# Optimization experiments

Hardware: AMD Instinct MI355X
Metric: run time of the kernel (lower is better)

Reference implementation:

```python
import jax, jax.numpy as jnp
import numpy as np

N = 50000      # nodes
E = 800000     # edges (avg degree 16)
D_IN, D_H, D_OUT = 128, 256, 128


def setup_inputs() -> dict:
    key = jax.random.key(0)
    ks = jax.random.split(key, 12)
    x = jax.random.normal(ks[0], (N, D_IN), jnp.float32)
    src = jax.random.randint(ks[1], (E,), 0, N)
    dst = jax.random.randint(ks[2], (E,), 0, N)

    def lin(k, din, dout):
        return (jax.random.normal(k, (din, dout), jnp.float32) / np.sqrt(din)).astype(jnp.float32)

    dims = [(D_IN, D_H), (D_H, D_H), (D_H, D_OUT)]
    params = {}
    ki = 3
    for i, (di, do) in enumerate(dims):
        params[f"W_self{i}"] = lin(ks[ki], di, do); ki += 1
        params[f"W_neigh{i}"] = lin(ks[ki], di, do); ki += 1
        params[f"b{i}"] = jnp.zeros((do,), jnp.float32)
    return {"x": x, "src": src, "dst": dst, **params}


def _mean_agg(h, src, dst):
    # gather src features along edges, segment-mean into dst nodes
    msg = jnp.take(h, src, axis=0)                              # [E, D]
    s = jax.ops.segment_sum(msg, dst, num_segments=N)           # [N, D]
    deg = jax.ops.segment_sum(jnp.ones((dst.shape[0], 1), h.dtype), dst, num_segments=N)
    return s / jnp.maximum(deg, 1.0)                            # zero-degree -> 0, as in DGL


def reference(x, src, dst,
              W_self0, W_neigh0, b0,
              W_self1, W_neigh1, b1,
              W_self2, W_neigh2, b2):
    Ws = [(W_self0, W_neigh0, b0), (W_self1, W_neigh1, b1), (W_self2, W_neigh2, b2)]
    h = x
    for i, (Ws_i, Wn_i, b_i) in enumerate(Ws):
        neigh = _mean_agg(h, src, dst)
        h = h @ Ws_i + neigh @ Wn_i + b_i                       # SAGEConv('mean')
        if i < len(Ws) - 1:
            h = jax.nn.relu(h)                                  # activation between layers
    return h
```

## Files before the change

### kernel.cpp

```cpp
#include <hip/hip_runtime.h>

#define NN 50000
#define NE 800000
#define NCHK 200
#define CHKE 4000
#define NBUK 196
#define BCAP 5120
#define NOFF (NBUK * NCHK)
#define NSB  ((NOFF + 255) / 256)

typedef __attribute__((ext_vector_type(8))) short short8;
typedef __attribute__((ext_vector_type(4))) float f32x4;
typedef unsigned int u32;
typedef unsigned short u16;

__device__ __forceinline__ float bf2f(short u) {
    union { unsigned int i; float f; } c;
    c.i = ((unsigned int)(unsigned short)u) << 16;
    return c.f;
}
__device__ __forceinline__ short f2bf(float f) {
    union { float f; unsigned int i; } c; c.f = f;
    unsigned int u = c.i;
    unsigned int r = (u + 0x7FFFu + ((u >> 16) & 1u)) >> 16;
    return (short)r;
}


__global__ void cvt_f32_bf16_kernel(const float* __restrict__ in, short* __restrict__ out, int n) {
    int gid = blockIdx.x * 256 + threadIdx.x;
    if (gid < n) out[gid] = f2bf(in[gid]);
}

__global__ void wcvt_all_kernel(const float* __restrict__ Ws0, const float* __restrict__ Wn0,
                                const float* __restrict__ Ws1, const float* __restrict__ Wn1,
                                const float* __restrict__ Ws2, const float* __restrict__ Wn2,
                                short* __restrict__ wts) {
    int gid = blockIdx.x * 256 + threadIdx.x;
    const float* W; int K, Dout, base, loc;
    if (gid < 65536)       { K = 128; Dout = 256; base = (gid < 32768)  ? 0 : 32768;
                             W = (gid < 32768)  ? Ws0 : Wn0; loc = gid & 32767; }
    else if (gid < 196608) { K = 256; Dout = 256; base = (gid < 131072) ? 65536 : 131072;
                             W = (gid < 131072) ? Ws1 : Wn1; loc = (gid - 65536) & 65535; }
    else                   { K = 256; Dout = 128; base = (gid < 229376) ? 196608 : 229376;
                             W = (gid < 229376) ? Ws2 : Wn2; loc = (gid - 196608) & 32767; }
    int k = loc / Dout, d = loc - k * Dout;
    int kt = k >> 6, ks = (k >> 5) & 1, kg = (k >> 3) & 3, j = k & 7;
    int cgp = d >> 4, l = d & 15;
    int off = ((((kt * 2 + ks) * (Dout >> 4) + cgp) * 4 + kg) * 16 + l) * 8 + j;
    wts[base + off] = f2bf(W[(long)k * Dout + d]);
}

__global__ __launch_bounds__(256) void bucket_hist_kernel(const int* __restrict__ dst,
                                                          int* __restrict__ chist) {
    __shared__ int lh[NBUK];
    int b = blockIdx.x, t = threadIdx.x;
    for (int i = t; i < NBUK; i += 256) lh[i] = 0;
    __syncthreads();
    int base = b * CHKE;
    for (int i = t; i < CHKE; i += 256) atomicAdd(&lh[dst[base + i] >> 8], 1);
    __syncthreads();
    for (int i = t; i < NBUK; i += 256) chist[i * NCHK + b] = lh[i];
}

__global__ __launch_bounds__(256) void off_blocksum_kernel(const int* __restrict__ in,
                                                           int* __restrict__ bsum) {
    __shared__ int sm[256];
    int t = threadIdx.x;
    int idx = blockIdx.x * 256 + t;
    sm[t] = (idx < NOFF) ? in[idx] : 0;
    __syncthreads();
    for (int off = 128; off > 0; off >>= 1) {
        if (t < off) sm[t] += sm[t + off];
        __syncthreads();
    }
    if (t == 0) bsum[blockIdx.x] = sm[0];
}

__global__ __launch_bounds__(256) void off_scanb_kernel(const int* __restrict__ bsum,
                                                        int* __restrict__ bpre) {
    __shared__ int sm[256];
    int t = threadIdx.x;
    sm[t] = (t < NSB) ? bsum[t] : 0;
    __syncthreads();
    for (int o = 1; o < 256; o <<= 1) {
        int v = sm[t];
        int a = (t >= o) ? sm[t - o] : 0;
        __syncthreads();
        sm[t] = v + a;
        __syncthreads();
    }
    if (t < NSB) bpre[t] = (t == 0) ? 0 : sm[t - 1];
}

__global__ __launch_bounds__(256) void off_scatter_kernel(const int* __restrict__ in,
                                                          const int* __restrict__ bpre,
                                                          int* __restrict__ off) {
    __shared__ int sm[256];
    int t = threadIdx.x;
    int idx = blockIdx.x * 256 + t;
    int val = (idx < NOFF) ? in[idx] : 0;
    sm[t] = val;
    __syncthreads();
    for (int o = 1; o < 256; o <<= 1) {
        int v = sm[t];
        int a = (t >= o) ? sm[t - o] : 0;
        __syncthreads();
        sm[t] = v + a;
        __syncthreads();
    }
    if (idx < NOFF) off[idx] = bpre[blockIdx.x] + sm[t] - val;
}

__global__ __launch_bounds__(256) void bucket_scatter_kernel(const int* __restrict__ src,
                                                             const int* __restrict__ dst,
                                                             const int* __restrict__ off,
                                                             u32* __restrict__ ebuf) {
    __shared__ int lcur[NBUK];
    int b = blockIdx.x, t = threadIdx.x;
    for (int i = t; i < NBUK; i += 256) lcur[i] = off[i * NCHK + b];
    __syncthreads();
    int base = b * CHKE;
    for (int i = t; i < CHKE; i += 256) {
        int d = dst[base + i], s = src[base + i];
        int slot = atomicAdd(&lcur[d >> 8], 1);
        ebuf[slot] = ((u32)(d & 255) << 16) | (u32)s;
    }
}

__global__ __launch_bounds__(256) void bucket_sort_kernel(const u32* __restrict__ ebuf,
                                                          const int* __restrict__ off,
                                                          u16* __restrict__ srcs16,
                                                          int* __restrict__ row_start,
                                                          int* __restrict__ cnt) {
    __shared__ u32 earr[BCAP];
    __shared__ u16 s16[BCAP];
    __shared__ int lhist[256], lpre[256], lcur[256];
    int k = blockIdx.x, t = threadIdx.x;
    int base = off[k * NCHK];
    int end  = (k < NBUK - 1) ? off[(k + 1) * NCHK] : NE;
    int nE = end - base;
    lhist[t] = 0;
    __syncthreads();
    for (int i = t; i < nE; i += 256) {
        u32 e = ebuf[base + i];
        earr[i] = e;
        atomicAdd(&lhist[e >> 16], 1);
    }
    __syncthreads();
    int v = lhist[t];
    lpre[t] = v;
    __syncthreads();
    for (int o = 1; o < 256; o <<= 1) {
        int x = lpre[t];
        int a = (t >= o) ? lpre[t - o] : 0;
        __syncthreads();
        lpre[t] = x + a;
        __syncthreads();
    }
    int excl = lpre[t] - v;
    int node = k * 256 + t;
    if (node < NN) { row_start[node] = base + excl; cnt[node] = v; }
    lcur[t] = excl;
    __syncthreads();
    for (int i = t; i < nE; i += 256) {
        u32 e = earr[i];
        int pos = atomicAdd(&lcur[e >> 16], 1);
        s16[pos] = (u16)(e & 0xFFFFu);
    }
    __syncthreads();
    for (int i = t; i < nE; i += 256) srcs16[base + i] = s16[i];
}


template<int STRIDE_G>
__global__ __launch_bounds__(256) void gather_mean3_kernel(
    const short* __restrict__ h, const u16* __restrict__ srcs,
    const int* __restrict__ row_start, const int* __restrict__ cnt,
    short* __restrict__ nb)
{
    constexpr int EPL = 4;
    const int wave = threadIdx.x >> 6;
    const int lane = threadIdx.x & 63;
    const int v = blockIdx.x * 4 + wave;
    if (v >= NN) return;
    const int go = blockIdx.y * 16;
    const int c  = cnt[v];
    const int rs = row_start[v];
    const int slot = lane >> 4;
    const int cg   = (lane & 15) + go;
    float acc[8];
    #pragma unroll
    for (int j = 0; j < 8; ++j) acc[j] = 0.f;
    const short8* hp = (const short8*)h;
    int i = slot;
    for (; i + 3 * EPL < c; i += 4 * EPL) {
        int s0 = srcs[rs + i];
        int s1 = srcs[rs + i + EPL];
        int s2 = srcs[rs + i + 2 * EPL];
        int s3 = srcs[rs + i + 3 * EPL];
        short8 v0 = hp[(size_t)s0 * STRIDE_G + cg];
        short8 v1 = hp[(size_t)s1 * STRIDE_G + cg];
        short8 v2 = hp[(size_t)s2 * STRIDE_G + cg];
        short8 v3 = hp[(size_t)s3 * STRIDE_G + cg];
        #pragma unroll
        for (int j = 0; j < 8; ++j)
            acc[j] += (bf2f(v0[j]) + bf2f(v1[j])) + (bf2f(v2[j]) + bf2f(v3[j]));
    }
    for (; i < c; i += EPL) {
        int s0 = srcs[rs + i];
        short8 v0 = hp[(size_t)s0 * STRIDE_G + cg];
        #pragma unroll
        for (int j = 0; j < 8; ++j) acc[j] += bf2f(v0[j]);
    }
    #pragma unroll
    for (int j = 0; j < 8; ++j) {
        acc[j] += __shfl_xor(acc[j], 16);
        acc[j] += __shfl_xor(acc[j], 32);
    }
    if (slot == 0) {
        float inv = (c > 0) ? (1.0f / (float)c) : 0.0f;
        short8 outv;
        #pragma unroll
        for (int j = 0; j < 8; ++j) outv[j] = f2bf(acc[j] * inv);
        ((short8*)nb)[(size_t)v * STRIDE_G + cg] = outv;
    }
}

template<int NOUT, int KK, int PHASES, bool RELU, bool OUT_F32, bool ADDIN, bool BIAS>
__global__ __launch_bounds__(256, 4) void gemm_sage5_kernel(
    const short* __restrict__ Aself, const short* __restrict__ Aneigh,
    const short* __restrict__ Bself, const short* __restrict__ Bneigh,
    const float* __restrict__ bias, void* __restrict__ outp, int M,
    const short* __restrict__ addin)
{
    constexpr int WN = NOUT / 64;
    constexpr int WM = 4 / WN;
    constexpr int BM = 64 * WM;
    constexpr int SC = BM / 32;
    constexpr int MR = 4;
    constexpr int NR = 4;
    constexpr int KT = KK / 64;
    constexpr int NT = PHASES * KT;
    constexpr int CG = NOUT / 16;

    __shared__ short ldsA[2][BM * 64];

    const int tid  = threadIdx.x;
    const int wave = tid >> 6;
    const int lane = tid & 63;
    const int wm = wave / WN;
    const int wn = wave % WN;
    const int l15 = lane & 15;
    const int kg  = lane >> 4;
    const int bm  = blockIdx.x * BM;

    f32x4 acc[MR][NR];
    #pragma unroll
    for (int a = 0; a < MR; ++a)
        #pragma unroll
        for (int b = 0; b < NR; ++b)
            acc[a][b] = (f32x4){0.f, 0.f, 0.f, 0.f};

    const int srow = tid >> 3;
    const int scol = ((tid & 7) << 3) ^ ((srow & 7) << 3);

    auto stageA = [&](int buf, int t) {
        int ph = t / KT, kt = t - ph * KT;
        const short* A = ph ? Aneigh : Aself;
        #pragma unroll
        for (int c = 0; c < SC; ++c) {
            const short* gp = A + (size_t)(bm + c * 32 + srow) * KK + kt * 64 + scol;
            __builtin_amdgcn_global_load_lds(
                (const __attribute__((address_space(1))) u32*)gp,
                (__attribute__((address_space(3))) u32*)(&ldsA[buf][c * 2048 + (wave << 9)]),
                16, 0, 0);
        }
    };

    stageA(0, 0);
    __syncthreads();

    for (int t = 0; t < NT; ++t) {
        const int cur = t & 1;
        if (t + 1 < NT) stageA(cur ^ 1, t + 1);
        const int ph = t / KT, kt = t - ph * KT;
        const short* __restrict__ Wb = ph ? Bneigh : Bself;

        #pragma unroll
        for (int ks = 0; ks < 2; ++ks) {
            short8 wreg[NR];
            #pragma unroll
            for (int nr = 0; nr < NR; ++nr)
                wreg[nr] = *(const short8*)(
                    Wb + (size_t)((((kt * 2 + ks) * CG + wn * NR + nr) * 4 + kg) * 16 + l15) * 8);
            short8 areg[MR];
            #pragma unroll
            for (int mr = 0; mr < MR; ++mr) {
                int r = wm * 64 + mr * 16 + l15;
                areg[mr] = *(const short8*)(&ldsA[cur][r * 64 + ((ks * 32 + kg * 8) ^ ((r & 7) << 3))]);
            }
            #pragma unroll
            for (int mr = 0; mr < MR; ++mr)
                #pragma unroll
                for (int nr = 0; nr < NR; ++nr)
                    acc[mr][nr] = __builtin_amdgcn_mfma_f32_16x16x32_bf16(
                        areg[mr], wreg[nr], acc[mr][nr], 0, 0, 0);
        }
        __syncthreads();
    }

    #pragma unroll
    for (int mr = 0; mr < MR; ++mr) {
        int rowb = bm + wm * 64 + mr * 16 + kg * 4;
        #pragma unroll
        for (int nr = 0; nr < NR; ++nr) {
            int col = wn * 64 + nr * 16 + l15;
            float bv = BIAS ? bias[col] : 0.f;
            #pragma unroll
            for (int r = 0; r < 4; ++r) {
                int row = rowb + r;
                if (row < M) {
                    float vv = acc[mr][nr][r] + bv;
                    if (ADDIN) vv += bf2f(addin[(size_t)row * NOUT + col]);
                    if (RELU) vv = fmaxf(vv, 0.f);
                    if (OUT_F32) ((float*)outp)[(size_t)row * NOUT + col] = vv;
                    else         ((short*)outp)[(size_t)row * NOUT + col] = f2bf(vv);
                }
            }
        }
    }
}


extern "C" void kernel_launch(void* const* d_in, const int* in_sizes, int n_in,
                              void* d_out, int out_size, void* d_ws, size_t ws_size,
                              hipStream_t stream) {
    const float* x    = (const float*)d_in[0];
    const int*   srcp = (const int*)d_in[1];
    const int*   dstp = (const int*)d_in[2];
    const float* Ws0  = (const float*)d_in[3];
    const float* Wn0  = (const float*)d_in[4];
    const float* b0   = (const float*)d_in[5];
    const float* Ws1  = (const float*)d_in[6];
    const float* Wn1  = (const float*)d_in[7];
    const float* b1   = (const float*)d_in[8];
    const float* Ws2  = (const float*)d_in[9];
    const float* Wn2  = (const float*)d_in[10];
    const float* b2   = (const float*)d_in[11];

    char* base = (char*)d_ws;
    size_t off_b = 0;
    auto alloc = [&](size_t bytes) -> void* {
        void* p = base + off_b;
        off_b += (bytes + 255) & ~(size_t)255;
        return p;
    };

    int*   cnt       = (int*)alloc((size_t)NN * 4);
    int*   row_start = (int*)alloc((size_t)NN * 4);
    int*   chist     = (int*)alloc((size_t)NOFF * 4);
    int*   offb      = (int*)alloc((size_t)NOFF * 4);
    int*   bsum      = (int*)alloc((size_t)NSB * 4);
    int*   bpre      = (int*)alloc((size_t)NSB * 4);
    u32*   ebuf      = (u32*)alloc((size_t)NE * 4);
    u16*   srcs16    = (u16*)alloc((size_t)NE * 2);
    short* hA        = (short*)alloc((size_t)NN * 256 * 2);
    short* hB        = (short*)alloc((size_t)NN * 256 * 2);
    short* nb        = (short*)alloc((size_t)NN * 256 * 2);
    short* wts       = (short*)alloc((size_t)262144 * 2 + 65536);
    short* Wt0s = wts;
    short* Wt0n = Wt0s + 32768;
    short* Wt1s = Wt0n + 32768;
    short* Wt1n = Wt1s + 65536;
    short* Wt2s = Wt1n + 65536;
    short* Wt2n = Wt2s + 32768;

    bucket_hist_kernel<<<NCHK, 256, 0, stream>>>(dstp, chist);
    off_blocksum_kernel<<<NSB, 256, 0, stream>>>(chist, bsum);
    off_scanb_kernel<<<1, 256, 0, stream>>>(bsum, bpre);
    off_scatter_kernel<<<NSB, 256, 0, stream>>>(chist, bpre, offb);
    bucket_scatter_kernel<<<NCHK, 256, 0, stream>>>(srcp, dstp, offb, ebuf);
    bucket_sort_kernel<<<NBUK, 256, 0, stream>>>(ebuf, offb, srcs16, row_start, cnt);

    wcvt_all_kernel<<<1024, 256, 0, stream>>>(Ws0, Wn0, Ws1, Wn1, Ws2, Wn2, wts);

    cvt_f32_bf16_kernel<<<(NN * 128 + 255) / 256, 256, 0, stream>>>(x, hA, NN * 128);

    const int mblk64  = (NN + 63) / 64;
    const int mblk128 = (NN + 127) / 128;
    const int gblocks = (NN + 3) / 4;

    gather_mean3_kernel<16><<<dim3(gblocks, 1), 256, 0, stream>>>(hA, srcs16, row_start, cnt, nb);
    gemm_sage5_kernel<256, 128, 2, true, false, false, true><<<mblk64, 256, 0, stream>>>(
        hA, nb, Wt0s, Wt0n, b0, hB, NN, nullptr);

    gather_mean3_kernel<32><<<dim3(gblocks, 2), 256, 0, stream>>>(hB, srcs16, row_start, cnt, nb);
    gemm_sage5_kernel<256, 256, 2, true, false, false, true><<<mblk64, 256, 0, stream>>>(
        hB, nb, Wt1s, Wt1n, b1, hA, NN, nullptr);

    gemm_sage5_kernel<128, 256, 1, false, false, false, false><<<mblk128, 256, 0, stream>>>(
        hA, hA, Wt2n, Wt2n, nullptr, hB, NN, nullptr);
    gather_mean3_kernel<16><<<dim3(gblocks, 1), 256, 0, stream>>>(hB, srcs16, row_start, cnt, nb);
    gemm_sage5_kernel<128, 256, 1, false, true, true, true><<<mblk128, 256, 0, stream>>>(
        hA, hA, Wt2s, Wt2s, b2, d_out, NN, nb);
}
```

Before: 236.2 us.

## Specialize gather kernels: full-row 256-wide waves and two nodes per wave for 128

Replaces the templated gather with two specialized kernels. For 256-wide features, one wave now covers the whole row with two edge slots and eight loads in flight, rather than splitting columns over two grid-y blocks. For 128-wide features, each wave processes two destination nodes at once, interleaving their loads to expose more memory-level parallelism. This aims to increase outstanding gather loads and cut the repeated index reads, at the cost of more registers and some tail imbalance.

```diff
diff --git a/kernel.cpp b/kernel.cpp
--- a/kernel.cpp
+++ b/kernel.cpp
@@ -172,58 +172,137 @@
     for (int i = t; i < nE; i += 256) srcs16[base + i] = s16[i];
 }
 
-
-template<int STRIDE_G>
-__global__ __launch_bounds__(256) void gather_mean3_kernel(
+__global__ __launch_bounds__(256) void gather256_kernel(
     const short* __restrict__ h, const u16* __restrict__ srcs,
     const int* __restrict__ row_start, const int* __restrict__ cnt,
     short* __restrict__ nb)
 {
-    constexpr int EPL = 4;
     const int wave = threadIdx.x >> 6;
     const int lane = threadIdx.x & 63;
     const int v = blockIdx.x * 4 + wave;
     if (v >= NN) return;
-    const int go = blockIdx.y * 16;
     const int c  = cnt[v];
     const int rs = row_start[v];
-    const int slot = lane >> 4;
-    const int cg   = (lane & 15) + go;
+    const int slot = lane >> 5;
+    const int cg   = lane & 31;
     float acc[8];
     #pragma unroll
     for (int j = 0; j < 8; ++j) acc[j] = 0.f;
     const short8* hp = (const short8*)h;
     int i = slot;
-    for (; i + 3 * EPL < c; i += 4 * EPL) {
-        int s0 = srcs[rs + i];
-        int s1 = srcs[rs + i + EPL];
-        int s2 = srcs[rs + i + 2 * EPL];
-        int s3 = srcs[rs + i + 3 * EPL];
-        short8 v0 = hp[(size_t)s0 * STRIDE_G + cg];
-        short8 v1 = hp[(size_t)s1 * STRIDE_G + cg];
-        short8 v2 = hp[(size_t)s2 * STRIDE_G + cg];
-        short8 v3 = hp[(size_t)s3 * STRIDE_G + cg];
-        #pragma unroll
-        for (int j = 0; j < 8; ++j)
-            acc[j] += (bf2f(v0[j]) + bf2f(v1[j])) + (bf2f(v2[j]) + bf2f(v3[j]));
-    }
-    for (; i < c; i += EPL) {
-        int s0 = srcs[rs + i];
-        short8 v0 = hp[(size_t)s0 * STRIDE_G + cg];
-        #pragma unroll
-        for (int j = 0; j < 8; ++j) acc[j] += bf2f(v0[j]);
-    }
-    #pragma unroll
-    for (int j = 0; j < 8; ++j) {
-        acc[j] += __shfl_xor(acc[j], 16);
-        acc[j] += __shfl_xor(acc[j], 32);
-    }
+    for (; i + 14 < c; i += 16) {
+        int s[8];
+        #pragma unroll
+        for (int u = 0; u < 8; ++u) s[u] = srcs[rs + i + 2 * u];
+        short8 r[8];
+        #pragma unroll
+        for (int u = 0; u < 8; ++u) r[u] = hp[(size_t)s[u] * 32 + cg];
+        #pragma unroll
+        for (int u = 0; u < 8; ++u)
+            #pragma unroll
+            for (int j = 0; j < 8; ++j) acc[j] += bf2f(r[u][j]);
+    }
+    for (; i < c; i += 2) {
+        short8 r0 = hp[(size_t)srcs[rs + i] * 32 + cg];
+        #pragma unroll
+        for (int j = 0; j < 8; ++j) acc[j] += bf2f(r0[j]);
+    }
+    #pragma unroll
+    for (int j = 0; j < 8; ++j) acc[j] += __shfl_xor(acc[j], 32);
     if (slot == 0) {
         float inv = (c > 0) ? (1.0f / (float)c) : 0.0f;
         short8 outv;
         #pragma unroll
         for (int j = 0; j < 8; ++j) outv[j] = f2bf(acc[j] * inv);
-        ((short8*)nb)[(size_t)v * STRIDE_G + cg] = outv;
+        ((short8*)nb)[(size_t)v * 32 + cg] = outv;
+    }
+}
+
+__global__ __launch_bounds__(256) void gather128_kernel(
+    const short* __restrict__ h, const u16* __restrict__ srcs,
+    const int* __restrict__ row_start, const int* __restrict__ cnt,
+    short* __restrict__ nb)
+{
+    const int wave = threadIdx.x >> 6;
+    const int lane = threadIdx.x & 63;
+    const int w = blockIdx.x * 4 + wave;
+    const int v0 = 2 * w, v1 = 2 * w + 1;
+    if (v0 >= NN) return;
+    const bool has1 = (v1 < NN);
+    const int c0 = cnt[v0], rs0 = row_start[v0];
+    const int c1 = has1 ? cnt[v1] : 0;
+    const int rs1 = has1 ? row_start[v1] : 0;
+    const int slot = lane >> 4;
+    const int cg   = lane & 15;
+    float a0[8], a1[8];
+    #pragma unroll
+    for (int j = 0; j < 8; ++j) { a0[j] = 0.f; a1[j] = 0.f; }
+    const short8* hp = (const short8*)h;
+    int i0 = slot, i1 = slot;
+    while (i0 + 12 < c0 && i1 + 12 < c1) {
+        int sa[4], sb[4];
+        #pragma unroll
+        for (int u = 0; u < 4; ++u) { sa[u] = srcs[rs0 + i0 + 4 * u]; sb[u] = srcs[rs1 + i1 + 4 * u]; }
+        short8 ra[4], rb[4];
+        #pragma unroll
+        for (int u = 0; u < 4; ++u) { ra[u] = hp[(size_t)sa[u] * 16 + cg]; rb[u] = hp[(size_t)sb[u] * 16 + cg]; }
+        #pragma unroll
+        for (int u = 0; u < 4; ++u)
+            #pragma unroll
+            for (int j = 0; j < 8; ++j) { a0[j] += bf2f(ra[u][j]); a1[j] += bf2f(rb[u][j]); }
+        i0 += 16; i1 += 16;
+    }
+    for (; i0 + 12 < c0; i0 += 16) {
+        int sa[4];
+        #pragma unroll
+        for (int u = 0; u < 4; ++u) sa[u] = srcs[rs0 + i0 + 4 * u];
+        short8 ra[4];
+        #pragma unroll
+        for (int u = 0; u < 4; ++u) ra[u] = hp[(size_t)sa[u] * 16 + cg];
+        #pragma unroll
+        for (int u = 0; u < 4; ++u)
+            #pragma unroll
+            for (int j = 0; j < 8; ++j) a0[j] += bf2f(ra[u][j]);
+    }
+    for (; i0 < c0; i0 += 4) {
+        short8 r0 = hp[(size_t)srcs[rs0 + i0] * 16 + cg];
+        #pragma unroll
+        for (int j = 0; j < 8; ++j) a0[j] += bf2f(r0[j]);
+    }
+    for (; i1 + 12 < c1; i1 += 16) {
+        int sb[4];
+        #pragma unroll
+        for (int u = 0; u < 4; ++u) sb[u] = srcs[rs1 + i1 + 4 * u];
+        short8 rb[4];
+        #pragma unroll
+        for (int u = 0; u < 4; ++u) rb[u] = hp[(size_t)sb[u] * 16 + cg];
+        #pragma unroll
+        for (int u = 0; u < 4; ++u)
+            #pragma unroll
+            for (int j = 0; j < 8; ++j) a1[j] += bf2f(rb[u][j]);
+    }
+    for (; i1 < c1; i1 += 4) {
+        short8 r1 = hp[(size_t)srcs[rs1 + i1] * 16 + cg];
+        #pragma unroll
+        for (int j = 0; j < 8; ++j) a1[j] += bf2f(r1[j]);
+    }
+    #pragma unroll
+    for (int j = 0; j < 8; ++j) {
+        a0[j] += __shfl_xor(a0[j], 16); a0[j] += __shfl_xor(a0[j], 32);
+        a1[j] += __shfl_xor(a1[j], 16); a1[j] += __shfl_xor(a1[j], 32);
+    }
+    if (slot == 0) {
+        float inv = (c0 > 0) ? (1.0f / (float)c0) : 0.0f;
+        short8 outv;
+        #pragma unroll
+        for (int j = 0; j < 8; ++j) outv[j] = f2bf(a0[j] * inv);
+        ((short8*)nb)[(size_t)v0 * 16 + cg] = outv;
+    } else if (slot == 1 && has1) {
+        float inv = (c1 > 0) ? (1.0f / (float)c1) : 0.0f;
+        short8 outv;
+        #pragma unroll
+        for (int j = 0; j < 8; ++j) outv[j] = f2bf(a1[j] * inv);
+        ((short8*)nb)[(size_t)v1 * 16 + cg] = outv;
     }
 }
 
@@ -389,19 +468,20 @@
 
     const int mblk64  = (NN + 63) / 64;
     const int mblk128 = (NN + 127) / 128;
-    const int gblocks = (NN + 3) / 4;
-
-    gather_mean3_kernel<16><<<dim3(gblocks, 1), 256, 0, stream>>>(hA, srcs16, row_start, cnt, nb);
+    const int g4 = (NN + 3) / 4;
+    const int g8 = (NN + 7) / 8;
+
+    gather128_kernel<<<g8, 256, 0, stream>>>(hA, srcs16, row_start, cnt, nb);
     gemm_sage5_kernel<256, 128, 2, true, false, false, true><<<mblk64, 256, 0, stream>>>(
         hA, nb, Wt0s, Wt0n, b0, hB, NN, nullptr);
 
-    gather_mean3_kernel<32><<<dim3(gblocks, 2), 256, 0, stream>>>(hB, srcs16, row_start, cnt, nb);
+    gather256_kernel<<<g4, 256, 0, stream>>>(hB, srcs16, row_start, cnt, nb);
     gemm_sage5_kernel<256, 256, 2, true, false, false, true><<<mblk64, 256, 0, stream>>>(
         hB, nb, Wt1s, Wt1n, b1, hA, NN, nullptr);
 
     gemm_sage5_kernel<128, 256, 1, false, false, false, false><<<mblk128, 256, 0, stream>>>(
         hA, hA, Wt2n, Wt2n, nullptr, hB, NN, nullptr);
-    gather_mean3_kernel<16><<<dim3(gblocks, 1), 256, 0, stream>>>(hB, srcs16, row_start, cnt, nb);
+    gather128_kernel<<<g8, 256, 0, stream>>>(hB, srcs16, row_start, cnt, nb);
     gemm_sage5_kernel<128, 256, 1, false, true, true, true><<<mblk128, 256, 0, stream>>>(
         hA, hA, Wt2s, Wt2s, b2, d_out, NN, nb);
 }
```

Result: slower. 242.3 us (+2.6%).

## Fuse mean-aggregation gather into SAGE GEMM kernel per 64-row tile

Applied to the files above, without the earlier changes.

Replaces the separate gather_mean3 kernels and the following GEMM launches with one fused kernel per layer. Each block first gathers and averages neighbor features for its 64 destination rows into nb, overlapping that work with an async global-to-LDS load of the first A tile. It then runs a double-buffered MFMA GEMM over self and neighbor inputs. The goal is fewer launches and reading nb while it is still in cache, at the cost of a serial gather phase inside each GEMM block (one lane group per node, no edge-slot parallelism) and lower gather parallelism.

```diff
diff --git a/kernel.cpp b/kernel.cpp
--- a/kernel.cpp
+++ b/kernel.cpp
@@ -172,58 +172,150 @@
     for (int i = t; i < nE; i += 256) srcs16[base + i] = s16[i];
 }
 
-
-template<int STRIDE_G>
-__global__ __launch_bounds__(256) void gather_mean3_kernel(
-    const short* __restrict__ h, const u16* __restrict__ srcs,
-    const int* __restrict__ row_start, const int* __restrict__ cnt,
-    short* __restrict__ nb)
+template<int NOUT, int KK, int GD, bool SAGE, bool RELU, bool OUT_F32>
+__global__ __launch_bounds__(256, 4) void sage_fused_kernel(
+    const short* __restrict__ A, const short* __restrict__ G,
+    const short* __restrict__ Bs, const short* __restrict__ Bn,
+    const float* __restrict__ bias, void* __restrict__ outp, int M,
+    const u16* __restrict__ srcs, const int* __restrict__ row_start,
+    const int* __restrict__ cnt, short* __restrict__ nb)
 {
-    constexpr int EPL = 4;
-    const int wave = threadIdx.x >> 6;
-    const int lane = threadIdx.x & 63;
-    const int v = blockIdx.x * 4 + wave;
-    if (v >= NN) return;
-    const int go = blockIdx.y * 16;
-    const int c  = cnt[v];
-    const int rs = row_start[v];
-    const int slot = lane >> 4;
-    const int cg   = (lane & 15) + go;
-    float acc[8];
+    constexpr int WN = NOUT / 64;
+    constexpr int WM = 4 / WN;
+    constexpr int MR = 64 / (WM * 16);
+    constexpr int NR = 4;
+    constexpr int KT = KK / 64;
+    constexpr int NT = (SAGE ? 2 : 1) * KT;
+    constexpr int CG = NOUT / 16;
+    constexpr int CPR = GD / 8;
+    constexpr int DPW = 64 / CPR;
+    constexpr int GITERS = 16 / DPW;
+
+    __shared__ short ldsA[2][64 * 64];
+
+    const int tid  = threadIdx.x;
+    const int wave = tid >> 6;
+    const int lane = tid & 63;
+    const int wm = wave / WN;
+    const int wn = wave % WN;
+    const int l15 = lane & 15;
+    const int kg  = lane >> 4;
+    const int bm  = blockIdx.x * 64;
+
+    const int srow = tid >> 3;
+    const int scol = ((tid & 7) << 3) ^ ((srow & 7) << 3);
+
+    auto stage = [&](const short* __restrict__ Ap, int buf, int kt) {
+        #pragma unroll
+        for (int c = 0; c < 2; ++c) {
+            const short* gp = Ap + (size_t)(bm + c * 32 + srow) * KK + kt * 64 + scol;
+            __builtin_amdgcn_global_load_lds(
+                (const __attribute__((address_space(1))) u32*)gp,
+                (__attribute__((address_space(3))) u32*)(&ldsA[buf][c * 2048 + (wave << 9)]),
+                16, 0, 0);
+        }
+    };
+
+    stage(A, 0, 0);
+
+    {
+        const int sub = lane / CPR;
+        const int cgi = lane % CPR;
+        const short8* hp = (const short8*)G;
+        #pragma unroll
+        for (int it = 0; it < GITERS; ++it) {
+            int v = bm + it * (4 * DPW) + wave * DPW + sub;
+            if (v < NN) {
+                const int c  = cnt[v];
+                const int rs = row_start[v];
+                float ac[8];
+                #pragma unroll
+                for (int j = 0; j < 8; ++j) ac[j] = 0.f;
+                int i = 0;
+                for (; i + 3 < c; i += 4) {
+                    int s0 = srcs[rs + i], s1 = srcs[rs + i + 1];
+                    int s2 = srcs[rs + i + 2], s3 = srcs[rs + i + 3];
+                    short8 r0 = hp[(size_t)s0 * CPR + cgi];
+                    short8 r1 = hp[(size_t)s1 * CPR + cgi];
+                    short8 r2 = hp[(size_t)s2 * CPR + cgi];
+                    short8 r3 = hp[(size_t)s3 * CPR + cgi];
+                    #pragma unroll
+                    for (int j = 0; j < 8; ++j)
+                        ac[j] += (bf2f(r0[j]) + bf2f(r1[j])) + (bf2f(r2[j]) + bf2f(r3[j]));
+                }
+                for (; i < c; ++i) {
+                    short8 r0 = hp[(size_t)srcs[rs + i] * CPR + cgi];
+                    #pragma unroll
+                    for (int j = 0; j < 8; ++j) ac[j] += bf2f(r0[j]);
+                }
+                float inv = (c > 0) ? (1.0f / (float)c) : 0.0f;
+                short8 outv;
+                #pragma unroll
+                for (int j = 0; j < 8; ++j) outv[j] = f2bf(ac[j] * inv);
+                ((short8*)nb)[(size_t)v * CPR + cgi] = outv;
+            }
+        }
+    }
+    __syncthreads();
+
+    f32x4 acc[MR][NR];
     #pragma unroll
-    for (int j = 0; j < 8; ++j) acc[j] = 0.f;
-    const short8* hp = (const short8*)h;
-    int i = slot;
-    for (; i + 3 * EPL < c; i += 4 * EPL) {
-        int s0 = srcs[rs + i];
-        int s1 = srcs[rs + i + EPL];
-        int s2 = srcs[rs + i + 2 * EPL];
-        int s3 = srcs[rs + i + 3 * EPL];
-        short8 v0 = hp[(size_t)s0 * STRIDE_G + cg];
-        short8 v1 = hp[(size_t)s1 * STRIDE_G + cg];
-        short8 v2 = hp[(size_t)s2 * STRIDE_G + cg];
-        short8 v3 = hp[(size_t)s3 * STRIDE_G + cg];
-        #pragma unroll
-        for (int j = 0; j < 8; ++j)
-            acc[j] += (bf2f(v0[j]) + bf2f(v1[j])) + (bf2f(v2[j]) + bf2f(v3[j]));
-    }
-    for (; i < c; i += EPL) {
-        int s0 = srcs[rs + i];
-        short8 v0 = hp[(size_t)s0 * STRIDE_G + cg];
-        #pragma unroll
-        for (int j = 0; j < 8; ++j) acc[j] += bf2f(v0[j]);
-    }
+    for (int a = 0; a < MR; ++a)
+        #pragma unroll
+        for (int b = 0; b < NR; ++b)
+            acc[a][b] = (f32x4){0.f, 0.f, 0.f, 0.f};
+
+    for (int t = 0; t < NT; ++t) {
+        const int cur = t & 1;
+        if (t + 1 < NT) {
+            const int np = (t + 1) / KT, nk = (t + 1) - np * KT;
+            stage(np ? nb : A, cur ^ 1, nk);
+        }
+        const int ph = t / KT, kt = t - ph * KT;
+        const short* __restrict__ Wb = ph ? Bn : Bs;
+
+        #pragma unroll
+        for (int ks = 0; ks < 2; ++ks) {
+            short8 wreg[NR];
+            #pragma unroll
+            for (int nr = 0; nr < NR; ++nr)
+                wreg[nr] = *(const short8*)(
+                    Wb + (size_t)((((kt * 2 + ks) * CG + wn * NR + nr) * 4 + kg) * 16 + l15) * 8);
+            short8 areg[MR];
+            #pragma unroll
+            for (int mr = 0; mr < MR; ++mr) {
+                int r = wm * (MR * 16) + mr * 16 + l15;
+                areg[mr] = *(const short8*)(&ldsA[cur][r * 64 + ((ks * 32 + kg * 8) ^ ((r & 7) << 3))]);
+            }
+            #pragma unroll
+            for (int mr = 0; mr < MR; ++mr)
+                #pragma unroll
+                for (int nr = 0; nr < NR; ++nr)
+                    acc[mr][nr] = __builtin_amdgcn_mfma_f32_16x16x32_bf16(
+                        areg[mr], wreg[nr], acc[mr][nr], 0, 0, 0);
+        }
+        __syncthreads();
+    }
+
     #pragma unroll
-    for (int j = 0; j < 8; ++j) {
-        acc[j] += __shfl_xor(acc[j], 16);
-        acc[j] += __shfl_xor(acc[j], 32);
-    }
-    if (slot == 0) {
-        float inv = (c > 0) ? (1.0f / (float)c) : 0.0f;
-        short8 outv;
-        #pragma unroll
-        for (int j = 0; j < 8; ++j) outv[j] = f2bf(acc[j] * inv);
-        ((short8*)nb)[(size_t)v * STRIDE_G + cg] = outv;
+    for (int mr = 0; mr < MR; ++mr) {
+        int rowb = bm + wm * (MR * 16) + mr * 16 + kg * 4;
+        #pragma unroll
+        for (int nr = 0; nr < NR; ++nr) {
+            int col = wn * 64 + nr * 16 + l15;
+            float bv = bias ? bias[col] : 0.f;
+            #pragma unroll
+            for (int r = 0; r < 4; ++r) {
+                int row = rowb + r;
+                if (row < M) {
+                    float vv = acc[mr][nr][r] + bv;
+                    if (!SAGE) vv += bf2f(nb[(size_t)row * NOUT + col]);
+                    if (RELU) vv = fmaxf(vv, 0.f);
+                    if (OUT_F32) ((float*)outp)[(size_t)row * NOUT + col] = vv;
+                    else         ((short*)outp)[(size_t)row * NOUT + col] = f2bf(vv);
+                }
+            }
+        }
     }
 }
 
@@ -368,7 +460,7 @@
     short* hA        = (short*)alloc((size_t)NN * 256 * 2);
     short* hB        = (short*)alloc((size_t)NN * 256 * 2);
     short* nb        = (short*)alloc((size_t)NN * 256 * 2);
-    short* wts       = (short*)alloc((size_t)262144 * 2 + 65536);
+    short* wts       = (short*)alloc((size_t)262144 * 2 + 131072);
     short* Wt0s = wts;
     short* Wt0n = Wt0s + 32768;
     short* Wt1s = Wt0n + 32768;
@@ -387,21 +479,17 @@
 
     cvt_f32_bf16_kernel<<<(NN * 128 + 255) / 256, 256, 0, stream>>>(x, hA, NN * 128);
 
-    const int mblk64  = (NN + 63) / 64;
+    const int fblk    = (NN + 63) / 64;
     const int mblk128 = (NN + 127) / 128;
-    const int gblocks = (NN + 3) / 4;
-
-    gather_mean3_kernel<16><<<dim3(gblocks, 1), 256, 0, stream>>>(hA, srcs16, row_start, cnt, nb);
-    gemm_sage5_kernel<256, 128, 2, true, false, false, true><<<mblk64, 256, 0, stream>>>(
-        hA, nb, Wt0s, Wt0n, b0, hB, NN, nullptr);
-
-    gather_mean3_kernel<32><<<dim3(gblocks, 2), 256, 0, stream>>>(hB, srcs16, row_start, cnt, nb);
-    gemm_sage5_kernel<256, 256, 2, true, false, false, true><<<mblk64, 256, 0, stream>>>(
-        hB, nb, Wt1s, Wt1n, b1, hA, NN, nullptr);
+
+    sage_fused_kernel<256, 128, 128, true, true, false><<<fblk, 256, 0, stream>>>(
+        hA, hA, Wt0s, Wt0n, b0, hB, NN, srcs16, row_start, cnt, nb);
+
+    sage_fused_kernel<256, 256, 256, true, true, false><<<fblk, 256, 0, stream>>>(
+        hB, hB, Wt1s, Wt1n, b1, hA, NN, srcs16, row_start, cnt, nb);
 
     gemm_sage5_kernel<128, 256, 1, false, false, false, false><<<mblk128, 256, 0, stream>>>(
         hA, hA, Wt2n, Wt2n, nullptr, hB, NN, nullptr);
-    gather_mean3_kernel<16><<<dim3(gblocks, 1), 256, 0, stream>>>(hB, srcs16, row_start, cnt, nb);
-    gemm_sage5_kernel<128, 256, 1, false, true, true, true><<<mblk128, 256, 0, stream>>>(
-        hA, hA, Wt2s, Wt2s, b2, d_out, NN, nb);
-}
+    sage_fused_kernel<128, 256, 128, false, false, true><<<fblk, 256, 0, stream>>>(
+        hA, hB, Wt2s, Wt2s, b2, d_out, NN, srcs16, row_start, cnt, nb);
+}
```

After: 241.3 us. 2.2% more time.
